# Kernel optimization log

Measured on AMD Instinct MI355X. Metric: run time of the kernel, lower is better.

The kernel has to match this reference:

```python
import jax, jax.numpy as jnp
import numpy as np

B, S, D = 4, 8192, 512


def setup_inputs() -> dict:
    key = jax.random.key(0)
    k1, k2, k3 = jax.random.split(key, 3)
    input_real = jax.random.normal(k1, (B, S, D), dtype=jnp.float32)
    input_imag = jax.random.normal(k2, (B, S, D), dtype=jnp.float32)
    weight = jax.random.uniform(k3, (B, S), dtype=jnp.float32)
    return {"input_real": input_real, "input_imag": input_imag, "weight": weight}


def reference(input_real, input_imag, weight):
    # Original: sum_s w[b,s] * (r_s r_s^T + i_s i_s^T)  and  sum_s w[b,s] * (i_s r_s^T - r_s i_s^T).
    # Algebraically equal to weighted Gram GEMMs X^T diag(w) Y; avoids the [B,S,D,D] intermediate.
    def wgram(x, y):
        # [B,S,D] x [B,S] x [B,S,D] -> [B,D,D]
        return jnp.einsum('bsd,bs,bse->bde', x, weight, y)

    output_r = wgram(input_real, input_real) + wgram(input_imag, input_imag)
    output_i = wgram(input_imag, input_real) - wgram(input_real, input_imag)
    return (output_r, output_i)
```

## Files before the change

kernel.cpp:

```cpp
#include <hip/hip_runtime.h>
#include <cstdint>
#include <cstddef>

#define NB 4
#define NS 8192
#define ND 512
#define NP 1024
#define BK 32

typedef __bf16 bf16x8 __attribute__((ext_vector_type(8)));
typedef float f32x4 __attribute__((ext_vector_type(4)));

union FragU { uint4 u; bf16x8 h; };

__device__ __forceinline__ void gload16(const void* g, void* l) {
  __builtin_amdgcn_global_load_lds(
      (const __attribute__((address_space(1))) unsigned int*)g,
      (__attribute__((address_space(3))) unsigned int*)l, 16, 0, 0);
}

__global__ __launch_bounds__(256)
void k_prep(const float* __restrict__ R, const float* __restrict__ I,
            const float* __restrict__ W, unsigned short* __restrict__ Yt) {
  __shared__ unsigned T[64][34];
  const int t   = threadIdx.x;
  const int blk = blockIdx.x;
  const int sb  = blk & 127;
  const int pb  = (blk >> 7) & 15;
  const int b   = blk >> 11;
  const float* src = (pb < 8) ? R : I;
  const int col0 = (pb & 7) * 64;
  const int s0 = sb * 64;
  const int c2 = t & 15;
  const int rp = t >> 4;
#pragma unroll
  for (int i = 0; i < 2; ++i) {
    const int r  = rp + 16 * i;
    const int sa = s0 + 2 * r;
    const float swa = sqrtf(W[b * NS + sa]);
    const float swb = sqrtf(W[b * NS + sa + 1]);
    const float4 va = *(const float4*)(src + (size_t)(b * NS + sa) * ND + col0 + c2 * 4);
    const float4 vb = *(const float4*)(src + (size_t)(b * NS + sa + 1) * ND + col0 + c2 * 4);
    unsigned p0, p1, p2, p3;
    asm("v_cvt_pk_bf16_f32 %0, %1, %2" : "=v"(p0) : "v"(va.x * swa), "v"(vb.x * swb));
    asm("v_cvt_pk_bf16_f32 %0, %1, %2" : "=v"(p1) : "v"(va.y * swa), "v"(vb.y * swb));
    asm("v_cvt_pk_bf16_f32 %0, %1, %2" : "=v"(p2) : "v"(va.z * swa), "v"(vb.z * swb));
    asm("v_cvt_pk_bf16_f32 %0, %1, %2" : "=v"(p3) : "v"(va.w * swa), "v"(vb.w * swb));
    T[c2 * 4 + 0][r] = p0;
    T[c2 * 4 + 1][r] = p1;
    T[c2 * 4 + 2][r] = p2;
    T[c2 * 4 + 3][r] = p3;
  }
  __syncthreads();
  const int sc = t & 7;
  const int d0 = t >> 3;
#pragma unroll
  for (int i = 0; i < 2; ++i) {
    const int d = d0 + 32 * i;
    uint4 o;
    o.x = T[d][sc * 4 + 0];
    o.y = T[d][sc * 4 + 1];
    o.z = T[d][sc * 4 + 2];
    o.w = T[d][sc * 4 + 3];
    *(uint4*)(Yt + (size_t)(b * NP + pb * 64 + d) * NS + s0 + sc * 8) = o;
  }
}

__global__ __launch_bounds__(512, 4)
void k_gemm(const unsigned short* __restrict__ Yt, float* __restrict__ part) {
  __shared__ uint4 lds4[4096];
  char* lds = (char*)lds4;
  static const int TMp[10] = {0,1,1,2,2,2,3,3,3,3};
  static const int TNp[10] = {0,0,1,0,1,2,0,1,2,3};
  const int bid = blockIdx.x;
  const int j   = (bid & 7) * 64 + (bid >> 3);
  const int g0 = j * 20;
  const int g1 = g0 + 20;
  const int p0 = g0 >> 8;
  const int p1 = (g1 - 1) >> 8;
  const int t = threadIdx.x;
  const int l = t & 63, w = t >> 6;

  const int cj = l & 7, jj = l >> 3;
  const int ec = cj ^ jj;
  const int rbase = w * 16 + 2 * jj + (ec >> 2);
  const int colo  = (ec & 3) * 8;
  int dstoff[4];
#pragma unroll
  for (int u = 0; u < 4; ++u) dstoff[u] = u * 8192 + w * 1024;

  const int gfr = l >> 4, e_ = l & 1, q = (l >> 1) & 7;
  const int ibase = ((l & 15) >> 1) * 128 + ((64 * e_ + 16 * gfr) ^ (q << 4));
  const int wm = w & 3, wn = w >> 2;
  const int mfb = wm * 2048;
  const int nfb = wn * 4096;
  const int lr = (l >> 4) * 4, lc = l & 15;

  for (int seg = 0; seg < 2; ++seg) {
    int pos, k0, ns;
    if (seg == 0) {
      pos = p0; k0 = g0 & 255;
      ns = 256 - k0; if (ns > 20) ns = 20;
    } else {
      if (p1 == p0) break;
      pos = p1; k0 = 0; ns = g1 & 255;
    }
    const int b = pos / 10, p = pos % 10;
    const int tm = TMp[p], tn = TNp[p];
    const int prow[4] = { tm * 128, 512 + tm * 128, tn * 128, 512 + tn * 128 };
    const unsigned short* gsrc[4];
#pragma unroll
    for (int u = 0; u < 4; ++u)
      gsrc[u] = Yt + (size_t)(b * NP + prow[u] + rbase) * NS
                + (size_t)k0 * BK + colo;

    f32x4 accr[2][4], acci[2][4];
    const f32x4 zz = {0.f, 0.f, 0.f, 0.f};
#pragma unroll
    for (int a = 0; a < 2; ++a)
#pragma unroll
      for (int c = 0; c < 4; ++c) { accr[a][c] = zz; acci[a][c] = zz; }

#pragma unroll
    for (int u = 0; u < 4; ++u) { gload16(gsrc[u], lds + dstoff[u]); gsrc[u] += BK; }
    __builtin_amdgcn_sched_barrier(0);
    asm volatile("s_waitcnt vmcnt(0)" ::: "memory");
    __builtin_amdgcn_s_barrier();

    int cur = 0;
    for (int ks = 0; ks < ns; ++ks) {
      const int cbase = cur * 32768;
      if (ks + 1 < ns) {
        const int nbase = cbase ^ 32768;
#pragma unroll
        for (int u = 0; u < 4; ++u) { gload16(gsrc[u], lds + nbase + dstoff[u]); gsrc[u] += BK; }
        __builtin_amdgcn_sched_barrier(0);
        asm volatile("s_waitcnt vmcnt(4)" ::: "memory");
      } else {
        asm volatile("s_waitcnt vmcnt(0)" ::: "memory");
      }
      __builtin_amdgcn_s_barrier();

      FragU ar[2], ai[2];
#pragma unroll
      for (int mf = 0; mf < 2; ++mf) {
        ar[mf].u = *(const uint4*)(lds + cbase +        mfb + mf * 1024 + ibase);
        ai[mf].u = *(const uint4*)(lds + cbase + 8192 + mfb + mf * 1024 + ibase);
      }
      __builtin_amdgcn_s_setprio(1);
#pragma unroll
      for (int nf = 0; nf < 4; ++nf) {
        FragU br, bi, bin;
        br.u = *(const uint4*)(lds + cbase + 16384 + nfb + nf * 1024 + ibase);
        bi.u = *(const uint4*)(lds + cbase + 24576 + nfb + nf * 1024 + ibase);
        bin.u.x = bi.u.x ^ 0x80008000u;
        bin.u.y = bi.u.y ^ 0x80008000u;
        bin.u.z = bi.u.z ^ 0x80008000u;
        bin.u.w = bi.u.w ^ 0x80008000u;
#pragma unroll
        for (int mf = 0; mf < 2; ++mf) {
          accr[mf][nf] = __builtin_amdgcn_mfma_f32_16x16x32_bf16(ar[mf].h, br.h,  accr[mf][nf], 0, 0, 0);
          accr[mf][nf] = __builtin_amdgcn_mfma_f32_16x16x32_bf16(ai[mf].h, bi.h,  accr[mf][nf], 0, 0, 0);
          acci[mf][nf] = __builtin_amdgcn_mfma_f32_16x16x32_bf16(ai[mf].h, br.h,  acci[mf][nf], 0, 0, 0);
          acci[mf][nf] = __builtin_amdgcn_mfma_f32_16x16x32_bf16(ar[mf].h, bin.h, acci[mf][nf], 0, 0, 0);
        }
      }
      __builtin_amdgcn_s_setprio(0);
      __builtin_amdgcn_s_barrier();
      cur ^= 1;
    }

    const int slot = (seg == 0) ? j : (512 + pos);
    const size_t baser = (size_t)slot * 32768;
    const size_t basei = baser + 16384;
#pragma unroll
    for (int mf = 0; mf < 2; ++mf)
#pragma unroll
      for (int nf = 0; nf < 4; ++nf)
#pragma unroll
        for (int r = 0; r < 4; ++r) {
          const int mi = wm * 32 + mf * 16 + lr + r;
          const int ni = wn * 64 + nf * 16 + lc;
          part[baser + (size_t)mi * 128 + ni] = accr[mf][nf][r];
          part[basei + (size_t)mi * 128 + ni] = acci[mf][nf][r];
        }
  }
}

__global__ __launch_bounds__(256)
void k_reduce(const float* __restrict__ part, float* __restrict__ out) {
  static const int TMp[10] = {0,1,1,2,2,2,3,3,3,3};
  static const int TNp[10] = {0,0,1,0,1,2,0,1,2,3};
  const int idx = blockIdx.x * 256 + threadIdx.x;
  const int n4 = idx & 31;
  const int mi = (idx >> 5) & 127;
  const int o  = (idx >> 12) & 1;
  const int P  = idx >> 13;
  const int jlo = (256 * P + 19) / 20;
  const int jhi = (256 * P + 255) / 20;
  const size_t off = (size_t)o * 16384 + (size_t)mi * 128 + n4 * 4;
  float4 a = {0.f, 0.f, 0.f, 0.f};
  for (int s = jlo; s <= jhi; ++s) {
    const float4 v = *(const float4*)(part + (size_t)s * 32768 + off);
    a.x += v.x; a.y += v.y; a.z += v.z; a.w += v.w;
  }
  if ((256 * P) % 20) {
    const float4 v = *(const float4*)(part + (size_t)(512 + P) * 32768 + off);
    a.x += v.x; a.y += v.y; a.z += v.z; a.w += v.w;
  }
  const int b = P / 10, p = P % 10;
  const int d = TMp[p] * 128 + mi;
  const int e = TNp[p] * 128 + n4 * 4;
  *(float4*)(out + (size_t)o * 1048576 + (size_t)b * 262144
             + (size_t)d * 512 + e) = a;
}

__global__ __launch_bounds__(256)
void k_mirror(float* __restrict__ out) {
  __shared__ float T[64][65];
  static const int UM[6] = {0,0,0,1,1,2};
  static const int UN[6] = {1,2,3,2,3,3};
  const int m = blockIdx.x;
  const int sub = m & 3;
  const int b   = (m >> 2) & 3;
  const int o   = (m >> 4) & 1;
  const int u   = m >> 5;
  const int d0 = UM[u] * 128 + (sub & 1) * 64;
  const int e0 = UN[u] * 128 + ((sub >> 1) & 1) * 64;
  const float sign = o ? -1.f : 1.f;
  float* base = out + (size_t)o * 1048576 + (size_t)b * 262144;
  const int t  = threadIdx.x;
  const int c4 = (t & 15) * 4;
  const int r0 = t >> 4;
#pragma unroll
  for (int i = 0; i < 4; ++i) {
    const int r = r0 + i * 16;
    const float4 v = *(const float4*)(base + (size_t)(e0 + r) * 512 + d0 + c4);
    T[c4 + 0][r] = v.x; T[c4 + 1][r] = v.y;
    T[c4 + 2][r] = v.z; T[c4 + 3][r] = v.w;
  }
  __syncthreads();
#pragma unroll
  for (int i = 0; i < 4; ++i) {
    const int r = r0 + i * 16;
    float4 wv;
    wv.x = sign * T[r][c4 + 0]; wv.y = sign * T[r][c4 + 1];
    wv.z = sign * T[r][c4 + 2]; wv.w = sign * T[r][c4 + 3];
    *(float4*)(base + (size_t)(d0 + r) * 512 + e0 + c4) = wv;
  }
}

__global__ __launch_bounds__(256)
void k_fallback(const float* __restrict__ R, const float* __restrict__ I,
                const float* __restrict__ W, float* __restrict__ out) {
  __shared__ float Rd[64][32], Id[64][32], Re[64][32], Ie[64][32];
  const int blk = blockIdx.x;
  const int et = blk & 15, dt = (blk >> 4) & 15, b = blk >> 8;
  const int d0 = dt * 32, e0 = et * 32;
  const int t = threadIdx.x;
  const int dd = t >> 3;
  const int ee0 = (t & 7) * 4;
  float ar[4] = {0,0,0,0}, ai[4] = {0,0,0,0};
  for (int s0 = 0; s0 < NS; s0 += 64) {
#pragma unroll
    for (int k = 0; k < 8; ++k) {
      const int idx = t + k * 256;
      const int row = idx >> 5, col = idx & 31;
      const float sw = sqrtf(W[b * NS + s0 + row]);
      const size_t gr = (size_t)(b * NS + s0 + row) * ND;
      Rd[row][col] = R[gr + d0 + col] * sw;
      Id[row][col] = I[gr + d0 + col] * sw;
      Re[row][col] = R[gr + e0 + col] * sw;
      Ie[row][col] = I[gr + e0 + col] * sw;
    }
    __syncthreads();
    for (int s = 0; s < 64; ++s) {
      const float rd = Rd[s][dd], id = Id[s][dd];
#pragma unroll
      for (int jx = 0; jx < 4; ++jx) {
        const float re = Re[s][ee0 + jx], ie = Ie[s][ee0 + jx];
        ar[jx] += rd * re + id * ie;
        ai[jx] += id * re - rd * ie;
      }
    }
    __syncthreads();
  }
  const size_t ob = (size_t)b * 262144;
#pragma unroll
  for (int jx = 0; jx < 4; ++jx) {
    out[          ob + (size_t)(d0 + dd) * 512 + e0 + ee0 + jx] = ar[jx];
    out[1048576 + ob + (size_t)(d0 + dd) * 512 + e0 + ee0 + jx] = ai[jx];
  }
}

extern "C" void kernel_launch(void* const* d_in, const int* in_sizes, int n_in,
                              void* d_out, int out_size, void* d_ws, size_t ws_size,
                              hipStream_t stream) {
  const float* R = (const float*)d_in[0];
  const float* I = (const float*)d_in[1];
  const float* W = (const float*)d_in[2];
  float* out = (float*)d_out;
  const size_t ytBytes   = (size_t)NB * NP * NS * 2;
  const size_t partBytes = (size_t)552 * 32768 * 4;

  if (ws_size < ytBytes + partBytes) {
    k_fallback<<<dim3(NB * 16 * 16), dim3(256), 0, stream>>>(R, I, W, out);
    return;
  }

  unsigned short* Yt = (unsigned short*)d_ws;
  float* part = (float*)((char*)d_ws + ytBytes);

  k_prep<<<dim3(NB * 16 * 128), dim3(256), 0, stream>>>(R, I, W, Yt);
  k_gemm<<<dim3(512), dim3(512), 0, stream>>>(Yt, part);
  k_reduce<<<dim3(1280), dim3(256), 0, stream>>>(part, out);
  k_mirror<<<dim3(192), dim3(256), 0, stream>>>(out);
}
```

Measured before the change: 229.0 us.

## Fuse mirror into reduce and enlarge prep tiles with swizzled LDS transpose

The separate mirror kernel is removed. The reduce kernel now writes each off-diagonal tile's transposed, sign-adjusted copy directly using scalar strided stores, which saves a launch and a re-read of the output. The prep kernel now handles 128 sequence rows per block, loads the weight pair as a float2, and uses an XOR-swizzled LDS layout for the transpose to cut bank conflicts. The trade-off is that the mirrored writes are uncoalesced 4-byte scatter stores.

```diff
diff --git a/kernel.cpp b/kernel.cpp
--- a/kernel.cpp
+++ b/kernel.cpp
@@ -22,23 +22,25 @@
 __global__ __launch_bounds__(256)
 void k_prep(const float* __restrict__ R, const float* __restrict__ I,
             const float* __restrict__ W, unsigned short* __restrict__ Yt) {
-  __shared__ unsigned T[64][34];
+  __shared__ unsigned T[64][68];
   const int t   = threadIdx.x;
   const int blk = blockIdx.x;
-  const int sb  = blk & 127;
-  const int pb  = (blk >> 7) & 15;
-  const int b   = blk >> 11;
+  const int sb  = blk & 63;
+  const int pb  = (blk >> 6) & 15;
+  const int b   = blk >> 10;
   const float* src = (pb < 8) ? R : I;
   const int col0 = (pb & 7) * 64;
-  const int s0 = sb * 64;
+  const int s0 = sb * 128;
   const int c2 = t & 15;
   const int rp = t >> 4;
-#pragma unroll
-  for (int i = 0; i < 2; ++i) {
-    const int r  = rp + 16 * i;
-    const int sa = s0 + 2 * r;
-    const float swa = sqrtf(W[b * NS + sa]);
-    const float swb = sqrtf(W[b * NS + sa + 1]);
+  const int key1 = 4 * (c2 >> 2);
+#pragma unroll
+  for (int i = 0; i < 4; ++i) {
+    const int pp = rp + 16 * i;
+    const int sa = s0 + 2 * pp;
+    const float2 w2 = *(const float2*)(W + b * NS + sa);
+    const float swa = sqrtf(w2.x);
+    const float swb = sqrtf(w2.y);
     const float4 va = *(const float4*)(src + (size_t)(b * NS + sa) * ND + col0 + c2 * 4);
     const float4 vb = *(const float4*)(src + (size_t)(b * NS + sa + 1) * ND + col0 + c2 * 4);
     unsigned p0, p1, p2, p3;
@@ -46,23 +48,25 @@
     asm("v_cvt_pk_bf16_f32 %0, %1, %2" : "=v"(p1) : "v"(va.y * swa), "v"(vb.y * swb));
     asm("v_cvt_pk_bf16_f32 %0, %1, %2" : "=v"(p2) : "v"(va.z * swa), "v"(vb.z * swb));
     asm("v_cvt_pk_bf16_f32 %0, %1, %2" : "=v"(p3) : "v"(va.w * swa), "v"(vb.w * swb));
-    T[c2 * 4 + 0][r] = p0;
-    T[c2 * 4 + 1][r] = p1;
-    T[c2 * 4 + 2][r] = p2;
-    T[c2 * 4 + 3][r] = p3;
+    const int col = pp ^ key1;
+    T[c2 * 4 + 0][col] = p0;
+    T[c2 * 4 + 1][col] = p1;
+    T[c2 * 4 + 2][col] = p2;
+    T[c2 * 4 + 3][col] = p3;
   }
   __syncthreads();
-  const int sc = t & 7;
-  const int d0 = t >> 3;
-#pragma unroll
-  for (int i = 0; i < 2; ++i) {
-    const int d = d0 + 32 * i;
+  const int c  = t & 15;
+  const int dr = t >> 4;
+#pragma unroll
+  for (int i = 0; i < 4; ++i) {
+    const int d = dr + 16 * i;
+    const int phys = (c * 4) ^ (4 * ((d >> 4) & 3));
     uint4 o;
-    o.x = T[d][sc * 4 + 0];
-    o.y = T[d][sc * 4 + 1];
-    o.z = T[d][sc * 4 + 2];
-    o.w = T[d][sc * 4 + 3];
-    *(uint4*)(Yt + (size_t)(b * NP + pb * 64 + d) * NS + s0 + sc * 8) = o;
+    o.x = T[d][phys + 0];
+    o.y = T[d][phys + 1];
+    o.z = T[d][phys + 2];
+    o.w = T[d][phys + 3];
+    *(uint4*)(Yt + (size_t)(b * NP + pb * 64 + d) * NS + s0 + c * 8) = o;
   }
 }
 
@@ -209,44 +213,17 @@
     a.x += v.x; a.y += v.y; a.z += v.z; a.w += v.w;
   }
   const int b = P / 10, p = P % 10;
-  const int d = TMp[p] * 128 + mi;
-  const int e = TNp[p] * 128 + n4 * 4;
-  *(float4*)(out + (size_t)o * 1048576 + (size_t)b * 262144
-             + (size_t)d * 512 + e) = a;
-}
-
-__global__ __launch_bounds__(256)
-void k_mirror(float* __restrict__ out) {
-  __shared__ float T[64][65];
-  static const int UM[6] = {0,0,0,1,1,2};
-  static const int UN[6] = {1,2,3,2,3,3};
-  const int m = blockIdx.x;
-  const int sub = m & 3;
-  const int b   = (m >> 2) & 3;
-  const int o   = (m >> 4) & 1;
-  const int u   = m >> 5;
-  const int d0 = UM[u] * 128 + (sub & 1) * 64;
-  const int e0 = UN[u] * 128 + ((sub >> 1) & 1) * 64;
-  const float sign = o ? -1.f : 1.f;
+  const int tm = TMp[p], tn = TNp[p];
+  const int d = tm * 128 + mi;
+  const int e = tn * 128 + n4 * 4;
   float* base = out + (size_t)o * 1048576 + (size_t)b * 262144;
-  const int t  = threadIdx.x;
-  const int c4 = (t & 15) * 4;
-  const int r0 = t >> 4;
-#pragma unroll
-  for (int i = 0; i < 4; ++i) {
-    const int r = r0 + i * 16;
-    const float4 v = *(const float4*)(base + (size_t)(e0 + r) * 512 + d0 + c4);
-    T[c4 + 0][r] = v.x; T[c4 + 1][r] = v.y;
-    T[c4 + 2][r] = v.z; T[c4 + 3][r] = v.w;
-  }
-  __syncthreads();
-#pragma unroll
-  for (int i = 0; i < 4; ++i) {
-    const int r = r0 + i * 16;
-    float4 wv;
-    wv.x = sign * T[r][c4 + 0]; wv.y = sign * T[r][c4 + 1];
-    wv.z = sign * T[r][c4 + 2]; wv.w = sign * T[r][c4 + 3];
-    *(float4*)(base + (size_t)(d0 + r) * 512 + e0 + c4) = wv;
+  *(float4*)(base + (size_t)d * 512 + e) = a;
+  if (tm != tn) {
+    const float sg = o ? -1.f : 1.f;
+    base[(size_t)(e + 0) * 512 + d] = sg * a.x;
+    base[(size_t)(e + 1) * 512 + d] = sg * a.y;
+    base[(size_t)(e + 2) * 512 + d] = sg * a.z;
+    base[(size_t)(e + 3) * 512 + d] = sg * a.w;
   }
 }
 
@@ -311,8 +288,7 @@
   unsigned short* Yt = (unsigned short*)d_ws;
   float* part = (float*)((char*)d_ws + ytBytes);
 
-  k_prep<<<dim3(NB * 16 * 128), dim3(256), 0, stream>>>(R, I, W, Yt);
+  k_prep<<<dim3(NB * 16 * 64), dim3(256), 0, stream>>>(R, I, W, Yt);
   k_gemm<<<dim3(512), dim3(512), 0, stream>>>(Yt, part);
   k_reduce<<<dim3(1280), dim3(256), 0, stream>>>(part, out);
-  k_mirror<<<dim3(192), dim3(256), 0, stream>>>(out);
-}
+}
```

Result: no change. 228.3 us (-0.3%).
